# Kernel tuning notes

Hardware: AMD Instinct MI355X
Metric: run time of the kernel (lower is better)

## Reference

```python
import jax, jax.numpy as jnp
import numpy as np

# dims
B, T, N, D = 4, 256, 64, 512
H, DH = 8, 64            # n_head, d_head; H*DH == D
DF = 4 * D               # SwiGLU hidden
EPS = 1e-6


def rmsnorm(x, w):
    return x * jax.lax.rsqrt(jnp.mean(x * x, axis=-1, keepdims=True) + EPS) * w


def phi(x):
    # positive feature map for kernelized (linear) attention ('SMReg' assumed elu+1 style)
    return jax.nn.elu(x) + 1.0


def heads(x):
    return x.reshape(*x.shape[:-1], H, DH)


def lin_att(Xq, Xkv, wq, wk, wv, wo):
    # low-rank high-order linear attention: kernelized attention applied
    # independently along each tensor mode (time T, entities N), averaged.
    q = phi(heads(Xq @ wq))   # [B,T,N,H,DH]
    k = phi(heads(Xkv @ wk))
    v = heads(Xkv @ wv)
    # mode 1 (time): attend over T, batch over (B,N)
    kv_t = jnp.einsum('btnhk,btnhv->bnhkv', k, v)          # [B,N,H,DH,DH]
    ks_t = k.sum(axis=1)                                   # [B,N,H,DH]
    den_t = jnp.einsum('btnhk,bnhk->btnh', q, ks_t) + EPS
    out_t = jnp.einsum('btnhk,bnhkv->btnhv', q, kv_t) / den_t[..., None]
    # mode 2 (entities): attend over N, batch over (B,T)
    kv_n = jnp.einsum('btnhk,btnhv->bthkv', k, v)
    ks_n = k.sum(axis=2)
    den_n = jnp.einsum('btnhk,bthk->btnh', q, ks_n) + EPS
    out_n = jnp.einsum('btnhk,bthkv->btnhv', q, kv_n) / den_n[..., None]
    out = 0.5 * (out_t + out_n)
    return out.reshape(*Xq.shape[:-1], H * DH) @ wo


def swiglu(x, w1, w2, w3):
    return (jax.nn.silu(x @ w1) * (x @ w3)) @ w2


def setup_inputs() -> dict:
    key = jax.random.key(0)
    ks = jax.random.split(key, 20)
    s = 0.02
    inp = {
        'X': jax.random.normal(ks[0], (B, T, N, D), jnp.float32),
        'Z': jax.random.normal(ks[1], (B, T, N, D), jnp.float32),
        'n1': jnp.ones((D,), jnp.float32),
        'n2': jnp.ones((D,), jnp.float32),
        'n3': jnp.ones((D,), jnp.float32),
        'nz': jnp.ones((D,), jnp.float32),
        'a_wq': jax.random.normal(ks[2], (D, H * DH), jnp.float32) * s,
        'a_wk': jax.random.normal(ks[3], (D, H * DH), jnp.float32) * s,
        'a_wv': jax.random.normal(ks[4], (D, H * DH), jnp.float32) * s,
        'a_wo': jax.random.normal(ks[5], (H * DH, D), jnp.float32) * s,
        'c_wq': jax.random.normal(ks[6], (D, H * DH), jnp.float32) * s,
        'c_wk': jax.random.normal(ks[7], (D, H * DH), jnp.float32) * s,
        'c_wv': jax.random.normal(ks[8], (D, H * DH), jnp.float32) * s,
        'c_wo': jax.random.normal(ks[9], (H * DH, D), jnp.float32) * s,
        'f_w1': jax.random.normal(ks[10], (D, DF), jnp.float32) * s,
        'f_w2': jax.random.normal(ks[11], (DF, D), jnp.float32) * s,
        'f_w3': jax.random.normal(ks[12], (D, DF), jnp.float32) * s,
    }
    return inp


def reference(X, Z, n1, n2, n3, nz, a_wq, a_wk, a_wv, a_wo,
              c_wq, c_wk, c_wv, c_wo, f_w1, f_w2, f_w3):
    # h = X + SelfAtt(norm1(X))
    xn = rmsnorm(X, n1)
    h = X + lin_att(xn, xn, a_wq, a_wk, a_wv, a_wo)
    # h = h + CrossAtt(norm3(h), normz(Z))
    h = h + lin_att(rmsnorm(h, n3), rmsnorm(Z, nz), c_wq, c_wk, c_wv, c_wo)
    # out = h + SwiGLU(norm2(h))   (dropout p=0 -> identity)
    return h + swiglu(rmsnorm(h, n2), f_w1, f_w2, f_w3)
```

## Files before the change

### kernel.cpp

```cpp
#include <hip/hip_runtime.h>

typedef short s16x8 __attribute__((ext_vector_type(8)));
typedef float f32x4 __attribute__((ext_vector_type(4)));
typedef unsigned short u16;
typedef unsigned int u32;

__device__ __forceinline__ float bf2f(u16 u) {
  union { unsigned int i; float f; } v; v.i = ((unsigned int)u) << 16; return v.f;
}
__device__ __forceinline__ u16 f2bf(float f) {
  union { float f; unsigned int i; } v; v.f = f;
  unsigned int r = v.i + 0x7fffu + ((v.i >> 16) & 1u);
  return (u16)(r >> 16);
}
__device__ __forceinline__ float bflo(u32 x) {
  union { unsigned int i; float f; } v; v.i = x << 16; return v.f;
}
__device__ __forceinline__ float bfhi(u32 x) {
  union { unsigned int i; float f; } v; v.i = x & 0xffff0000u; return v.f;
}

__device__ __forceinline__ void gload16(const u16* g, u16* l) {
  __builtin_amdgcn_global_load_lds(
      (const __attribute__((address_space(1))) u32*)g,
      (__attribute__((address_space(3))) u32*)l, 16, 0, 0);
}

template<int KDIM, int NDIM>
__launch_bounds__(256)
__global__ void wprep(const float* __restrict__ in, u16* __restrict__ out) {
  __shared__ float t[64][65];
  const int tid = threadIdx.x;
  const int nb = NDIM / 64;
  const int tk0 = (blockIdx.x / nb) * 64;
  const int tn0 = (blockIdx.x % nb) * 64;
#pragma unroll
  for (int i = 0; i < 16; i++) {
    int idx = i * 256 + tid;
    int r = idx >> 6, c = idx & 63;
    t[r][c] = in[(long)(tk0 + r) * NDIM + (tn0 + c)];
  }
  __syncthreads();
#pragma unroll
  for (int i = 0; i < 16; i++) {
    int idx = i * 256 + tid;
    int nn = idx >> 6, kk = idx & 63;
    out[(long)(tn0 + nn) * KDIM + (tk0 + kk)] = f2bf(t[kk][nn]);
  }
}

__launch_bounds__(256)
__global__ void rmsnorm_f32(const float* __restrict__ x, const float* __restrict__ w,
                            u16* __restrict__ out) {
  const long row = (long)blockIdx.x * 4 + (threadIdx.x >> 6);
  const int lane = threadIdx.x & 63;
  const float* xr = x + row * 512 + lane * 8;
  float4 v0 = *(const float4*)xr;
  float4 v1 = *(const float4*)(xr + 4);
  float ss = v0.x*v0.x + v0.y*v0.y + v0.z*v0.z + v0.w*v0.w
           + v1.x*v1.x + v1.y*v1.y + v1.z*v1.z + v1.w*v1.w;
#pragma unroll
  for (int o = 1; o < 64; o <<= 1) ss += __shfl_xor(ss, o);
  float sc = rsqrtf(ss * (1.0f / 512.0f) + 1e-6f);
  const float* wp = w + lane * 8;
  float4 w0 = *(const float4*)wp;
  float4 w1 = *(const float4*)(wp + 4);
  union { u16 u[8]; uint4 v; } o;
  o.u[0] = f2bf(v0.x * sc * w0.x);
  o.u[1] = f2bf(v0.y * sc * w0.y);
  o.u[2] = f2bf(v0.z * sc * w0.z);
  o.u[3] = f2bf(v0.w * sc * w0.w);
  o.u[4] = f2bf(v1.x * sc * w1.x);
  o.u[5] = f2bf(v1.y * sc * w1.y);
  o.u[6] = f2bf(v1.z * sc * w1.z);
  o.u[7] = f2bf(v1.w * sc * w1.w);
  *(uint4*)(out + row * 512 + lane * 8) = o.v;
}

__launch_bounds__(256)
__global__ void rmsnorm_bf16(const u16* __restrict__ x, const float* __restrict__ w,
                             u16* __restrict__ out) {
  const long row = (long)blockIdx.x * 4 + (threadIdx.x >> 6);
  const int lane = threadIdx.x & 63;
  uint4 u = *(const uint4*)(x + row * 512 + lane * 8);
  const u16* us = (const u16*)&u;
  float f[8];
  float ss = 0.f;
#pragma unroll
  for (int j = 0; j < 8; j++) { f[j] = bf2f(us[j]); ss += f[j] * f[j]; }
#pragma unroll
  for (int o = 1; o < 64; o <<= 1) ss += __shfl_xor(ss, o);
  float sc = rsqrtf(ss * (1.0f / 512.0f) + 1e-6f);
  const float* wp = w + lane * 8;
  union { u16 u[8]; uint4 v; } o;
#pragma unroll
  for (int j = 0; j < 8; j++) o.u[j] = f2bf(f[j] * sc * wp[j]);
  *(uint4*)(out + row * 512 + lane * 8) = o.v;
}

enum { EPI_BF16 = 0, EPI_PHI = 1, EPI_RESX = 2, EPI_RESH = 3, EPI_SILUMUL = 4,
       EPI_OUTF = 5, EPI_QKV = 6, EPI_KV = 7 };

template<int KD, int EPI>
__launch_bounds__(256)
__global__ void gemm128(const u16* __restrict__ A, const u16* __restrict__ Bt,
                        void* __restrict__ C0, void* __restrict__ C1,
                        void* __restrict__ C2, const void* __restrict__ aux,
                        int Ns) {
  __shared__ u16 smem[32768];
  u16* Asm = smem;
  u16* Bsm = smem + 16384;
  const int tid = threadIdx.x;
  const int lane = tid & 63;
  const int wv = tid >> 6;
  const int gx = gridDim.x;
  int L = blockIdx.y * gx + blockIdx.x;
  const int cpx = (gx * gridDim.y) >> 3;
  L = (L & 7) * cpx + (L >> 3);
  const long m0 = (long)(L / gx) * 128;
  const int nb = L % gx;
  const long n0 = (long)nb * 128;

  const int wr = (wv >> 1) * 64;
  const int wc = (wv & 1) * 64;
  const int fr = lane & 15;
  const int frq = lane >> 4;

  const int r0 = wv * 32 + (lane >> 3);
  const int sg8 = ((lane & 7) ^ ((lane >> 3) & 7)) * 8;
  const u16* Ag = A + (m0 + r0) * KD + sg8;
  const u16* Bg = Bt + (n0 + r0) * KD + sg8;
  u16* Alds = Asm + wv * 2048;
  u16* Blds = Bsm + wv * 2048;

  f32x4 acc[4][4] = {};

  auto STAGE = [&](int b, int kt) {
    const long k0 = (long)kt * 64;
#pragma unroll
    for (int j = 0; j < 4; j++) {
      gload16(Ag + (long)(j * 8) * KD + k0, Alds + b * 8192 + j * 512);
      gload16(Bg + (long)(j * 8) * KD + k0, Blds + b * 8192 + j * 512);
    }
  };
  auto COMPUTE = [&](int b) {
#pragma unroll
    for (int ks = 0; ks < 2; ks++) {
      const int slot = ((ks * 4 + frq) ^ (fr & 7)) * 8;
      s16x8 af[4], bf[4];
#pragma unroll
      for (int i = 0; i < 4; i++)
        af[i] = *(const s16x8*)&Asm[b * 8192 + (wr + i * 16 + fr) * 64 + slot];
#pragma unroll
      for (int j = 0; j < 4; j++)
        bf[j] = *(const s16x8*)&Bsm[b * 8192 + (wc + j * 16 + fr) * 64 + slot];
#pragma unroll
      for (int i = 0; i < 4; i++)
#pragma unroll
        for (int j = 0; j < 4; j++)
          acc[i][j] = __builtin_amdgcn_mfma_f32_16x16x32_bf16(af[i], bf[j], acc[i][j], 0, 0, 0);
    }
  };

  constexpr int NT = KD / 64;
  STAGE(0, 0);
#pragma unroll 1
  for (int t = 0; t < NT; ++t) {
    if (t + 1 < NT) {
      STAGE((t + 1) & 1, t + 1);
      asm volatile("s_waitcnt vmcnt(8)" ::: "memory");
    } else {
      asm volatile("s_waitcnt vmcnt(0)" ::: "memory");
    }
    __builtin_amdgcn_s_barrier();
    COMPUTE(t & 1);
    asm volatile("s_waitcnt lgkmcnt(0)" ::: "memory");
    __builtin_amdgcn_s_barrier();
  }

  u16* Cs = smem;
  const int col = lane & 15;
  const int rb = frq * 4;
  const int seg = (EPI == EPI_QKV || EPI == EPI_KV) ? (nb >> 2) : 0;
#pragma unroll
  for (int i = 0; i < 4; i++) {
#pragma unroll
    for (int r = 0; r < 4; r++) {
      const int ml = wr + i * 16 + rb + r;
#pragma unroll
      for (int j = 0; j < 4; j++) {
        const int nl = wc + j * 16 + col;
        float v = acc[i][j][r];
        if constexpr (EPI == EPI_PHI) {
          v = v > 0.f ? v + 1.f : __expf(v);
        } else if constexpr (EPI == EPI_QKV) {
          if (seg < 2) v = v > 0.f ? v + 1.f : __expf(v);
        } else if constexpr (EPI == EPI_KV) {
          if (seg == 0) v = v > 0.f ? v + 1.f : __expf(v);
        }
        Cs[ml * 148 + nl] = f2bf(v);
      }
    }
  }
  __syncthreads();

#pragma unroll
  for (int rep = 0; rep < 8; rep++) {
    const int idx = rep * 256 + tid;
    const int row = idx >> 4;
    const int nc = (idx & 15) * 8;
    const long m = m0 + row;
    uint4 vv = *(const uint4*)&Cs[row * 148 + nc];
    const u16* vp = (const u16*)&vv;
    if constexpr (EPI == EPI_QKV) {
      u16* P = (u16*)(seg == 0 ? C0 : (seg == 1 ? C1 : C2));
      *(uint4*)(P + m * 512 + (int)((n0 + nc) & 511)) = vv;
    } else if constexpr (EPI == EPI_KV) {
      u16* P = (u16*)(seg == 0 ? C0 : C1);
      *(uint4*)(P + m * 512 + (int)((n0 + nc) & 511)) = vv;
    } else if constexpr (EPI == EPI_BF16 || EPI == EPI_PHI) {
      *(uint4*)((u16*)C0 + m * Ns + n0 + nc) = vv;
    } else if constexpr (EPI == EPI_RESX) {
      const float* ax = (const float*)aux + m * Ns + n0 + nc;
      float4 a0 = *(const float4*)ax;
      float4 a1 = *(const float4*)(ax + 4);
      union { u16 u[8]; uint4 v; } o;
      o.u[0] = f2bf(a0.x + bf2f(vp[0]));
      o.u[1] = f2bf(a0.y + bf2f(vp[1]));
      o.u[2] = f2bf(a0.z + bf2f(vp[2]));
      o.u[3] = f2bf(a0.w + bf2f(vp[3]));
      o.u[4] = f2bf(a1.x + bf2f(vp[4]));
      o.u[5] = f2bf(a1.y + bf2f(vp[5]));
      o.u[6] = f2bf(a1.z + bf2f(vp[6]));
      o.u[7] = f2bf(a1.w + bf2f(vp[7]));
      *(uint4*)((u16*)C0 + m * Ns + n0 + nc) = o.v;
    } else if constexpr (EPI == EPI_RESH) {
      uint4 hh = *(const uint4*)((const u16*)aux + m * Ns + n0 + nc);
      const u16* hp = (const u16*)&hh;
      union { u16 u[8]; uint4 v; } o;
#pragma unroll
      for (int e = 0; e < 8; e++) o.u[e] = f2bf(bf2f(hp[e]) + bf2f(vp[e]));
      *(uint4*)((u16*)C0 + m * Ns + n0 + nc) = o.v;
    } else if constexpr (EPI == EPI_SILUMUL) {
      uint4 tt = *(const uint4*)((const u16*)aux + m * Ns + n0 + nc);
      const u16* tp = (const u16*)&tt;
      union { u16 u[8]; uint4 v; } o;
#pragma unroll
      for (int e = 0; e < 8; e++) {
        float t2 = bf2f(tp[e]);
        float s = t2 / (1.f + __expf(-t2));
        o.u[e] = f2bf(s * bf2f(vp[e]));
      }
      *(uint4*)((u16*)C0 + m * Ns + n0 + nc) = o.v;
    } else {
      uint4 hh = *(const uint4*)((const u16*)aux + m * Ns + n0 + nc);
      const u16* hp = (const u16*)&hh;
      float* o = (float*)C0 + m * Ns + n0 + nc;
      float4 o0, o1;
      o0.x = bf2f(hp[0]) + bf2f(vp[0]);
      o0.y = bf2f(hp[1]) + bf2f(vp[1]);
      o0.z = bf2f(hp[2]) + bf2f(vp[2]);
      o0.w = bf2f(hp[3]) + bf2f(vp[3]);
      o1.x = bf2f(hp[4]) + bf2f(vp[4]);
      o1.y = bf2f(hp[5]) + bf2f(vp[5]);
      o1.z = bf2f(hp[6]) + bf2f(vp[6]);
      o1.w = bf2f(hp[7]) + bf2f(vp[7]);
      *(float4*)o = o0;
      *(float4*)(o + 4) = o1;
    }
  }
}

__launch_bounds__(256)
__global__ void att_mode1(const u16* __restrict__ q, const u16* __restrict__ k,
                          const u16* __restrict__ v, u16* __restrict__ attc) {
  __shared__ u32 KT[64][132];
  __shared__ u32 VT[64][132];
  __shared__ u16 KVT[64][72];
  __shared__ float ksump[4][64];
  __shared__ float ksum_s[64];
  __shared__ float dinv[256];
  const int tid = threadIdx.x;
  const int lane = tid & 63;
  const int w = tid >> 6;
  const int bnh = blockIdx.x;
  const int h = bnh & 7;
  const int bn = bnh >> 3;
  const int n = bn & 63;
  const int b = bn >> 6;
  const long base = ((long)b * 16384 + n) * 512 + h * 64;
  const int fr = lane & 15;
  const int frq = lane >> 4;
  const int fk = frq * 8;

#pragma unroll
  for (int r = 0; r < 4; r++) {
    const int tp = (tid & 63) + (r & 1) * 64;
    const int c8 = (tid >> 6) + (r >> 1) * 4;
    const long g0 = base + (long)(2 * tp) * 32768 + c8 * 8;
    uint4 ka = *(const uint4*)(k + g0);
    uint4 kb = *(const uint4*)(k + g0 + 32768);
    uint4 va = *(const uint4*)(v + g0);
    uint4 vb = *(const uint4*)(v + g0 + 32768);
    const u16* kap = (const u16*)&ka; const u16* kbp = (const u16*)&kb;
    const u16* vap = (const u16*)&va; const u16* vbp = (const u16*)&vb;
#pragma unroll
    for (int e = 0; e < 8; e++) {
      KT[c8 * 8 + e][tp] = (u32)kap[e] | ((u32)kbp[e] << 16);
      VT[c8 * 8 + e][tp] = (u32)vap[e] | ((u32)vbp[e] << 16);
    }
  }
  __syncthreads();

  {
    const int dk = tid >> 2, qq = tid & 3;
    float s = 0.f;
#pragma unroll
    for (int i = 0; i < 8; i++) {
      uint4 x = *(const uint4*)&KT[dk][qq * 32 + i * 4];
      s += bflo(x.x) + bfhi(x.x) + bflo(x.y) + bfhi(x.y)
         + bflo(x.z) + bfhi(x.z) + bflo(x.w) + bfhi(x.w);
    }
    ksump[qq][dk] = s;
  }

  f32x4 acc[4] = {};
#pragma unroll
  for (int ks = 0; ks < 8; ks++) {
    s16x8 af = *(const s16x8*)&VT[w * 16 + fr][ks * 16 + frq * 4];
    s16x8 bk[4];
#pragma unroll
    for (int j = 0; j < 4; j++)
      bk[j] = *(const s16x8*)&KT[j * 16 + fr][ks * 16 + frq * 4];
#pragma unroll
    for (int j = 0; j < 4; j++)
      acc[j] = __builtin_amdgcn_mfma_f32_16x16x32_bf16(af, bk[j], acc[j], 0, 0, 0);
  }
  __syncthreads();
  {
    const int colL = lane & 15, rb = frq * 4;
#pragma unroll
    for (int j = 0; j < 4; j++)
#pragma unroll
      for (int r = 0; r < 4; r++)
        KVT[w * 16 + rb + r][j * 16 + colL] = f2bf(acc[j][r]);
  }
  if (tid < 64) ksum_s[tid] = ksump[0][tid] + ksump[1][tid] + ksump[2][tid] + ksump[3][tid];
  __syncthreads();
  {
    const u16* qp = q + base + (long)tid * 32768;
    float d = 0.f;
#pragma unroll
    for (int c8 = 0; c8 < 8; c8++) {
      uint4 u = ((const uint4*)qp)[c8];
      const u16* us = (const u16*)&u;
#pragma unroll
      for (int e = 0; e < 8; e++) d += bf2f(us[e]) * ksum_s[c8 * 8 + e];
    }
    dinv[tid] = 0.5f / (d + 1e-6f);
  }
  f32x4 acc2[4][4] = {};
#pragma unroll
  for (int ks = 0; ks < 2; ks++) {
    s16x8 aq[4], bk[4];
#pragma unroll
    for (int i = 0; i < 4; i++)
      aq[i] = *(const s16x8*)(q + base + (long)(w * 64 + i * 16 + fr) * 32768 + ks * 32 + fk);
#pragma unroll
    for (int j = 0; j < 4; j++)
      bk[j] = *(const s16x8*)&KVT[j * 16 + fr][ks * 32 + fk];
#pragma unroll
    for (int i = 0; i < 4; i++)
#pragma unroll
      for (int j = 0; j < 4; j++)
        acc2[i][j] = __builtin_amdgcn_mfma_f32_16x16x32_bf16(aq[i], bk[j], acc2[i][j], 0, 0, 0);
  }
  __syncthreads();
  const int colL = lane & 15, rb = frq * 4;
#pragma unroll
  for (int i = 0; i < 4; i++)
#pragma unroll
    for (int r = 0; r < 4; r++) {
      int t = w * 64 + i * 16 + rb + r;
      float inv = dinv[t];
#pragma unroll
      for (int j = 0; j < 4; j++)
        attc[base + (long)t * 32768 + j * 16 + colL] = f2bf(acc2[i][j][r] * inv);
    }
}

__launch_bounds__(256)
__global__ void att_mode2(const u16* __restrict__ q, const u16* __restrict__ k,
                          const u16* __restrict__ v, u16* __restrict__ attc) {
  __shared__ u32 KT[64][36];
  __shared__ u32 VT[64][36];
  __shared__ u16 KVT[64][72];
  __shared__ float ksump[4][64];
  __shared__ float ksum_s[64];
  __shared__ float dinv[64];
  const int tid = threadIdx.x;
  const int lane = tid & 63;
  const int w = tid >> 6;
  const int bth = blockIdx.x;
  const int h = bth & 7;
  const long bt = bth >> 3;
  const long base = bt * 32768 + h * 64;
  const int fr = lane & 15;
  const int frq = lane >> 4;
  const int fk = frq * 8;

  {
    const int np = tid & 31;
    const int c8 = tid >> 5;
    const long g0 = base + (long)(2 * np) * 512 + c8 * 8;
    uint4 ka = *(const uint4*)(k + g0);
    uint4 kb = *(const uint4*)(k + g0 + 512);
    uint4 va = *(const uint4*)(v + g0);
    uint4 vb = *(const uint4*)(v + g0 + 512);
    const u16* kap = (const u16*)&ka; const u16* kbp = (const u16*)&kb;
    const u16* vap = (const u16*)&va; const u16* vbp = (const u16*)&vb;
#pragma unroll
    for (int e = 0; e < 8; e++) {
      KT[c8 * 8 + e][np] = (u32)kap[e] | ((u32)kbp[e] << 16);
      VT[c8 * 8 + e][np] = (u32)vap[e] | ((u32)vbp[e] << 16);
    }
  }
  __syncthreads();
  {
    const int dk = tid >> 2, qq = tid & 3;
    uint4 x0 = *(const uint4*)&KT[dk][qq * 8];
    uint4 x1 = *(const uint4*)&KT[dk][qq * 8 + 4];
    float s = bflo(x0.x) + bfhi(x0.x) + bflo(x0.y) + bfhi(x0.y)
            + bflo(x0.z) + bfhi(x0.z) + bflo(x0.w) + bfhi(x0.w)
            + bflo(x1.x) + bfhi(x1.x) + bflo(x1.y) + bfhi(x1.y)
            + bflo(x1.z) + bfhi(x1.z) + bflo(x1.w) + bfhi(x1.w);
    ksump[qq][dk] = s;
  }
  f32x4 acc[4] = {};
#pragma unroll
  for (int ks = 0; ks < 2; ks++) {
    s16x8 af = *(const s16x8*)&VT[w * 16 + fr][ks * 16 + frq * 4];
    s16x8 bk[4];
#pragma unroll
    for (int j = 0; j < 4; j++)
      bk[j] = *(const s16x8*)&KT[j * 16 + fr][ks * 16 + frq * 4];
#pragma unroll
    for (int j = 0; j < 4; j++)
      acc[j] = __builtin_amdgcn_mfma_f32_16x16x32_bf16(af, bk[j], acc[j], 0, 0, 0);
  }
  __syncthreads();
  {
    const int colL = lane & 15, rb = frq * 4;
#pragma unroll
    for (int j = 0; j < 4; j++)
#pragma unroll
      for (int r = 0; r < 4; r++)
        KVT[w * 16 + rb + r][j * 16 + colL] = f2bf(acc[j][r]);
  }
  if (tid < 64) ksum_s[tid] = ksump[0][tid] + ksump[1][tid] + ksump[2][tid] + ksump[3][tid];
  __syncthreads();
  if (tid < 64) {
    const u16* qp = q + base + (long)tid * 512;
    float d = 0.f;
#pragma unroll
    for (int c8 = 0; c8 < 8; c8++) {
      uint4 u = ((const uint4*)qp)[c8];
      const u16* us = (const u16*)&u;
#pragma unroll
      for (int e = 0; e < 8; e++) d += bf2f(us[e]) * ksum_s[c8 * 8 + e];
    }
    dinv[tid] = 0.5f / (d + 1e-6f);
  }
  f32x4 acc2[4] = {};
#pragma unroll
  for (int ks = 0; ks < 2; ks++) {
    s16x8 aq, bk[4];
    aq = *(const s16x8*)(q + base + (long)(w * 16 + fr) * 512 + ks * 32 + fk);
#pragma unroll
    for (int j = 0; j < 4; j++)
      bk[j] = *(const s16x8*)&KVT[j * 16 + fr][ks * 32 + fk];
#pragma unroll
    for (int j = 0; j < 4; j++)
      acc2[j] = __builtin_amdgcn_mfma_f32_16x16x32_bf16(aq, bk[j], acc2[j], 0, 0, 0);
  }
  __syncthreads();
  const int colL = lane & 15, rb = frq * 4;
#pragma unroll
  for (int r = 0; r < 4; r++) {
    int nr = w * 16 + rb + r;
    float inv = dinv[nr];
#pragma unroll
    for (int j = 0; j < 4; j++) {
      long o = base + (long)nr * 512 + j * 16 + colL;
      attc[o] = f2bf(bf2f(attc[o]) + acc2[j][r] * inv);
    }
  }
}

extern "C" void kernel_launch(void* const* d_in, const int* in_sizes, int n_in,
                              void* d_out, int out_size, void* d_ws, size_t ws_size,
                              hipStream_t stream) {
  const float* X    = (const float*)d_in[0];
  const float* Z    = (const float*)d_in[1];
  const float* n1   = (const float*)d_in[2];
  const float* n2   = (const float*)d_in[3];
  const float* n3   = (const float*)d_in[4];
  const float* nz   = (const float*)d_in[5];
  const float* a_wq = (const float*)d_in[6];
  const float* a_wk = (const float*)d_in[7];
  const float* a_wv = (const float*)d_in[8];
  const float* a_wo = (const float*)d_in[9];
  const float* c_wq = (const float*)d_in[10];
  const float* c_wk = (const float*)d_in[11];
  const float* c_wv = (const float*)d_in[12];
  const float* c_wo = (const float*)d_in[13];
  const float* f_w1 = (const float*)d_in[14];
  const float* f_w2 = (const float*)d_in[15];
  const float* f_w3 = (const float*)d_in[16];
  float* out = (float*)d_out;
  (void)ws_size; (void)in_sizes; (void)n_in; (void)out_size;

  char* p = (char*)d_ws;
  size_t off = 0;
  auto take = [&](size_t bytes) -> char* {
    char* r = p + off;
    off += (bytes + 255) & ~(size_t)255;
    return r;
  };
  u16* w_aq = (u16*)take(512 * 512 * 2);
  u16* w_ak = (u16*)take(512 * 512 * 2);
  u16* w_av = (u16*)take(512 * 512 * 2);
  u16* w_ao = (u16*)take(512 * 512 * 2);
  u16* w_cq = (u16*)take(512 * 512 * 2);
  u16* w_ck = (u16*)take(512 * 512 * 2);
  u16* w_cv = (u16*)take(512 * 512 * 2);
  u16* w_co = (u16*)take(512 * 512 * 2);
  u16* w_f1 = (u16*)take(2048 * 512 * 2);
  u16* w_f3 = (u16*)take(2048 * 512 * 2);
  u16* w_f2 = (u16*)take(512 * 2048 * 2);
  u16* xn   = (u16*)take((size_t)65536 * 512 * 2);
  u16* hbuf = (u16*)take((size_t)65536 * 512 * 2);
  u16* qbuf = (u16*)take((size_t)65536 * 512 * 2);
  u16* kbuf = (u16*)d_out;
  u16* vbuf = (u16*)d_out + (size_t)65536 * 512;
  u16* attc = xn;
  u16* tslot = qbuf;

  dim3 b256(256);
  dim3 gQKV(12, 512);
  dim3 gKV(8, 512);
  dim3 gP(4, 512);
  dim3 gU(16, 128);
  dim3 gD(4, 128);

  wprep<512, 512><<<64, b256, 0, stream>>>(a_wq, w_aq);
  wprep<512, 512><<<64, b256, 0, stream>>>(a_wk, w_ak);
  wprep<512, 512><<<64, b256, 0, stream>>>(a_wv, w_av);
  wprep<512, 512><<<64, b256, 0, stream>>>(a_wo, w_ao);
  wprep<512, 512><<<64, b256, 0, stream>>>(c_wq, w_cq);
  wprep<512, 512><<<64, b256, 0, stream>>>(c_wk, w_ck);
  wprep<512, 512><<<64, b256, 0, stream>>>(c_wv, w_cv);
  wprep<512, 512><<<64, b256, 0, stream>>>(c_wo, w_co);
  wprep<512, 2048><<<256, b256, 0, stream>>>(f_w1, w_f1);
  wprep<512, 2048><<<256, b256, 0, stream>>>(f_w3, w_f3);
  wprep<2048, 512><<<256, b256, 0, stream>>>(f_w2, w_f2);

  rmsnorm_f32<<<16384, b256, 0, stream>>>(X, n1, xn);
  gemm128<512, EPI_QKV><<<gQKV, b256, 0, stream>>>(xn, w_aq, qbuf, kbuf, vbuf, nullptr, 1536);
  att_mode1<<<2048, b256, 0, stream>>>(qbuf, kbuf, vbuf, attc);
  att_mode2<<<8192, b256, 0, stream>>>(qbuf, kbuf, vbuf, attc);
  gemm128<512, EPI_RESX><<<gP, b256, 0, stream>>>(attc, w_ao, hbuf, nullptr, nullptr, X, 512);

  rmsnorm_bf16<<<16384, b256, 0, stream>>>(hbuf, n3, xn);
  gemm128<512, EPI_PHI><<<gP, b256, 0, stream>>>(xn, w_cq, qbuf, nullptr, nullptr, nullptr, 512);
  rmsnorm_f32<<<16384, b256, 0, stream>>>(Z, nz, xn);
  gemm128<512, EPI_KV><<<gKV, b256, 0, stream>>>(xn, w_ck, kbuf, vbuf, nullptr, nullptr, 1024);
  att_mode1<<<2048, b256, 0, stream>>>(qbuf, kbuf, vbuf, attc);
  att_mode2<<<8192, b256, 0, stream>>>(qbuf, kbuf, vbuf, attc);
  gemm128<512, EPI_RESH><<<gP, b256, 0, stream>>>(attc, w_co, hbuf, nullptr, nullptr, hbuf, 512);

  rmsnorm_bf16<<<16384, b256, 0, stream>>>(hbuf, n2, xn);
  const int CH = 16384;
  for (int c = 0; c < 4; c++) {
    const size_t ro = (size_t)c * CH * 512;
    gemm128<512, EPI_BF16><<<gU, b256, 0, stream>>>(xn + ro, w_f1, tslot, nullptr, nullptr, nullptr, 2048);
    gemm128<512, EPI_SILUMUL><<<gU, b256, 0, stream>>>(xn + ro, w_f3, tslot, nullptr, nullptr, tslot, 2048);
    gemm128<2048, EPI_OUTF><<<gD, b256, 0, stream>>>(tslot, w_f2, out + ro, nullptr, nullptr, hbuf + ro, 512);
  }
}
```

Measured before the change: 1.432 ms.

## Halve GEMM shared memory with K=32 stages and two-pass epilogue for occupancy

```diff
diff --git a/kernel.cpp b/kernel.cpp
--- a/kernel.cpp
+++ b/kernel.cpp
@@ -102,14 +102,12 @@
        EPI_OUTF = 5, EPI_QKV = 6, EPI_KV = 7 };
 
 template<int KD, int EPI>
-__launch_bounds__(256)
+__launch_bounds__(256, 5)
 __global__ void gemm128(const u16* __restrict__ A, const u16* __restrict__ Bt,
                         void* __restrict__ C0, void* __restrict__ C1,
                         void* __restrict__ C2, const void* __restrict__ aux,
                         int Ns) {
-  __shared__ u16 smem[32768];
-  u16* Asm = smem;
-  u16* Bsm = smem + 16384;
+  __shared__ u16 smem[16384];
   const int tid = threadIdx.x;
   const int lane = tid & 63;
   const int wv = tid >> 6;
@@ -126,49 +124,50 @@
   const int fr = lane & 15;
   const int frq = lane >> 4;
 
-  const int r0 = wv * 32 + (lane >> 3);
-  const int sg8 = ((lane & 7) ^ ((lane >> 3) & 7)) * 8;
-  const u16* Ag = A + (m0 + r0) * KD + sg8;
-  const u16* Bg = Bt + (n0 + r0) * KD + sg8;
-  u16* Alds = Asm + wv * 2048;
-  u16* Blds = Bsm + wv * 2048;
+  const int sig = (lane & 7) ^ ((lane >> 3) & 7);
+  const int grow = wv * 32 + 2 * (lane >> 3) + (sig >> 2);
+  const u16* Ag = A + (m0 + grow) * KD + (sig & 3) * 8;
+  const u16* Bg = Bt + (n0 + grow) * KD + (sig & 3) * 8;
 
   f32x4 acc[4][4] = {};
 
   auto STAGE = [&](int b, int kt) {
-    const long k0 = (long)kt * 64;
-#pragma unroll
-    for (int j = 0; j < 4; j++) {
-      gload16(Ag + (long)(j * 8) * KD + k0, Alds + b * 8192 + j * 512);
-      gload16(Bg + (long)(j * 8) * KD + k0, Blds + b * 8192 + j * 512);
-    }
+    const long k0 = (long)kt * 32;
+    gload16(Ag + k0, smem + b * 4096 + wv * 1024);
+    gload16(Ag + (long)16 * KD + k0, smem + b * 4096 + wv * 1024 + 512);
+    gload16(Bg + k0, smem + 8192 + b * 4096 + wv * 1024);
+    gload16(Bg + (long)16 * KD + k0, smem + 8192 + b * 4096 + wv * 1024 + 512);
   };
   auto COMPUTE = [&](int b) {
-#pragma unroll
-    for (int ks = 0; ks < 2; ks++) {
-      const int slot = ((ks * 4 + frq) ^ (fr & 7)) * 8;
-      s16x8 af[4], bf[4];
-#pragma unroll
-      for (int i = 0; i < 4; i++)
-        af[i] = *(const s16x8*)&Asm[b * 8192 + (wr + i * 16 + fr) * 64 + slot];
+    s16x8 af[4], bf[4];
+#pragma unroll
+    for (int i = 0; i < 4; i++) {
+      const int r = wr + i * 16 + fr;
+      const int pr = r >> 1;
+      const int sl = (((r & 1) * 4 + frq) ^ (pr & 7)) * 8;
+      af[i] = *(const s16x8*)&smem[b * 4096 + pr * 64 + sl];
+    }
+#pragma unroll
+    for (int j = 0; j < 4; j++) {
+      const int r = wc + j * 16 + fr;
+      const int pr = r >> 1;
+      const int sl = (((r & 1) * 4 + frq) ^ (pr & 7)) * 8;
+      bf[j] = *(const s16x8*)&smem[8192 + b * 4096 + pr * 64 + sl];
+    }
+#pragma unroll
+    for (int i = 0; i < 4; i++)
 #pragma unroll
       for (int j = 0; j < 4; j++)
-        bf[j] = *(const s16x8*)&Bsm[b * 8192 + (wc + j * 16 + fr) * 64 + slot];
-#pragma unroll
-      for (int i = 0; i < 4; i++)
-#pragma unroll
-        for (int j = 0; j < 4; j++)
-          acc[i][j] = __builtin_amdgcn_mfma_f32_16x16x32_bf16(af[i], bf[j], acc[i][j], 0, 0, 0);
-    }
+        acc[i][j] = __builtin_amdgcn_mfma_f32_16x16x32_bf16(af[i], bf[j], acc[i][j], 0, 0, 0);
   };
 
-  constexpr int NT = KD / 64;
+  constexpr int NT = KD / 32;
   STAGE(0, 0);
 #pragma unroll 1
   for (int t = 0; t < NT; ++t) {
     if (t + 1 < NT) {
       STAGE((t + 1) & 1, t + 1);
-      asm volatile("s_waitcnt vmcnt(8)" ::: "memory");
+      asm volatile("s_waitcnt vmcnt(4)" ::: "memory");
     } else {
       asm volatile("s_waitcnt vmcnt(0)" ::: "memory");
     }
@@ -183,91 +182,96 @@
   const int rb = frq * 4;
   const int seg = (EPI == EPI_QKV || EPI == EPI_KV) ? (nb >> 2) : 0;
 #pragma unroll
-  for (int i = 0; i < 4; i++) {
-#pragma unroll
-    for (int r = 0; r < 4; r++) {
-      const int ml = wr + i * 16 + rb + r;
-#pragma unroll
-      for (int j = 0; j < 4; j++) {
-        const int nl = wc + j * 16 + col;
-        float v = acc[i][j][r];
-        if constexpr (EPI == EPI_PHI) {
-          v = v > 0.f ? v + 1.f : __expf(v);
-        } else if constexpr (EPI == EPI_QKV) {
-          if (seg < 2) v = v > 0.f ? v + 1.f : __expf(v);
-        } else if constexpr (EPI == EPI_KV) {
-          if (seg == 0) v = v > 0.f ? v + 1.f : __expf(v);
+  for (int hh = 0; hh < 2; ++hh) {
+    if ((wv >> 1) == hh) {
+#pragma unroll
+      for (int i = 0; i < 4; i++) {
+#pragma unroll
+        for (int r = 0; r < 4; r++) {
+          const int mloc = i * 16 + rb + r;
+#pragma unroll
+          for (int j = 0; j < 4; j++) {
+            const int nl = wc + j * 16 + col;
+            float v = acc[i][j][r];
+            if constexpr (EPI == EPI_PHI) {
+              v = v > 0.f ? v + 1.f : __expf(v);
+            } else if constexpr (EPI == EPI_QKV) {
+              if (seg < 2) v = v > 0.f ? v + 1.f : __expf(v);
+            } else if constexpr (EPI == EPI_KV) {
+              if (seg == 0) v = v > 0.f ? v + 1.f : __expf(v);
+            }
+            Cs[mloc * 132 + nl] = f2bf(v);
+          }
         }
-        Cs[ml * 148 + nl] = f2bf(v);
       }
     }
-  }
-  __syncthreads();
-
-#pragma unroll
-  for (int rep = 0; rep < 8; rep++) {
-    const int idx = rep * 256 + tid;
-    const int row = idx >> 4;
-    const int nc = (idx & 15) * 8;
-    const long m = m0 + row;
-    uint4 vv = *(const uint4*)&Cs[row * 148 + nc];
-    const u16* vp = (const u16*)&vv;
-    if constexpr (EPI == EPI_QKV) {
-      u16* P = (u16*)(seg == 0 ? C0 : (seg == 1 ? C1 : C2));
-      *(uint4*)(P + m * 512 + (int)((n0 + nc) & 511)) = vv;
-    } else if constexpr (EPI == EPI_KV) {
-      u16* P = (u16*)(seg == 0 ? C0 : C1);
-      *(uint4*)(P + m * 512 + (int)((n0 + nc) & 511)) = vv;
-    } else if constexpr (EPI == EPI_BF16 || EPI == EPI_PHI) {
-      *(uint4*)((u16*)C0 + m * Ns + n0 + nc) = vv;
-    } else if constexpr (EPI == EPI_RESX) {
-      const float* ax = (const float*)aux + m * Ns + n0 + nc;
-      float4 a0 = *(const float4*)ax;
-      float4 a1 = *(const float4*)(ax + 4);
-      union { u16 u[8]; uint4 v; } o;
-      o.u[0] = f2bf(a0.x + bf2f(vp[0]));
-      o.u[1] = f2bf(a0.y + bf2f(vp[1]));
-      o.u[2] = f2bf(a0.z + bf2f(vp[2]));
-      o.u[3] = f2bf(a0.w + bf2f(vp[3]));
-      o.u[4] = f2bf(a1.x + bf2f(vp[4]));
-      o.u[5] = f2bf(a1.y + bf2f(vp[5]));
-      o.u[6] = f2bf(a1.z + bf2f(vp[6]));
-      o.u[7] = f2bf(a1.w + bf2f(vp[7]));
-      *(uint4*)((u16*)C0 + m * Ns + n0 + nc) = o.v;
-    } else if constexpr (EPI == EPI_RESH) {
-      uint4 hh = *(const uint4*)((const u16*)aux + m * Ns + n0 + nc);
-      const u16* hp = (const u16*)&hh;
-      union { u16 u[8]; uint4 v; } o;
-#pragma unroll
-      for (int e = 0; e < 8; e++) o.u[e] = f2bf(bf2f(hp[e]) + bf2f(vp[e]));
-      *(uint4*)((u16*)C0 + m * Ns + n0 + nc) = o.v;
-    } else if constexpr (EPI == EPI_SILUMUL) {
-      uint4 tt = *(const uint4*)((const u16*)aux + m * Ns + n0 + nc);
-      const u16* tp = (const u16*)&tt;
-      union { u16 u[8]; uint4 v; } o;
-#pragma unroll
-      for (int e = 0; e < 8; e++) {
-        float t2 = bf2f(tp[e]);
-        float s = t2 / (1.f + __expf(-t2));
-        o.u[e] = f2bf(s * bf2f(vp[e]));
+    __syncthreads();
+#pragma unroll
+    for (int rep = 0; rep < 4; rep++) {
+      const int idx = rep * 256 + tid;
+      const int row = idx >> 4;
+      const int nc = (idx & 15) * 8;
+      const long m = m0 + hh * 64 + row;
+      uint4 vv = *(const uint4*)&Cs[row * 132 + nc];
+      const u16* vp = (const u16*)&vv;
+      if constexpr (EPI == EPI_QKV) {
+        u16* P = (u16*)(seg == 0 ? C0 : (seg == 1 ? C1 : C2));
+        *(uint4*)(P + m * 512 + (int)((n0 + nc) & 511)) = vv;
+      } else if constexpr (EPI == EPI_KV) {
+        u16* P = (u16*)(seg == 0 ? C0 : C1);
+        *(uint4*)(P + m * 512 + (int)((n0 + nc) & 511)) = vv;
+      } else if constexpr (EPI == EPI_BF16 || EPI == EPI_PHI) {
+        *(uint4*)((u16*)C0 + m * Ns + n0 + nc) = vv;
+      } else if constexpr (EPI == EPI_RESX) {
+        const float* ax = (const float*)aux + m * Ns + n0 + nc;
+        float4 a0 = *(const float4*)ax;
+        float4 a1 = *(const float4*)(ax + 4);
+        union { u16 u[8]; uint4 v; } o;
+        o.u[0] = f2bf(a0.x + bf2f(vp[0]));
+        o.u[1] = f2bf(a0.y + bf2f(vp[1]));
+        o.u[2] = f2bf(a0.z + bf2f(vp[2]));
+        o.u[3] = f2bf(a0.w + bf2f(vp[3]));
+        o.u[4] = f2bf(a1.x + bf2f(vp[4]));
+        o.u[5] = f2bf(a1.y + bf2f(vp[5]));
+        o.u[6] = f2bf(a1.z + bf2f(vp[6]));
+        o.u[7] = f2bf(a1.w + bf2f(vp[7]));
+        *(uint4*)((u16*)C0 + m * Ns + n0 + nc) = o.v;
+      } else if constexpr (EPI == EPI_RESH) {
+        uint4 hhv = *(const uint4*)((const u16*)aux + m * Ns + n0 + nc);
+        const u16* hp = (const u16*)&hhv;
+        union { u16 u[8]; uint4 v; } o;
+#pragma unroll
+        for (int e = 0; e < 8; e++) o.u[e] = f2bf(bf2f(hp[e]) + bf2f(vp[e]));
+        *(uint4*)((u16*)C0 + m * Ns + n0 + nc) = o.v;
+      } else if constexpr (EPI == EPI_SILUMUL) {
+        uint4 tt = *(const uint4*)((const u16*)aux + m * Ns + n0 + nc);
+        const u16* tp = (const u16*)&tt;
+        union { u16 u[8]; uint4 v; } o;
+#pragma unroll
+        for (int e = 0; e < 8; e++) {
+          float t2 = bf2f(tp[e]);
+          float s = t2 / (1.f + __expf(-t2));
+          o.u[e] = f2bf(s * bf2f(vp[e]));
+        }
+        *(uint4*)((u16*)C0 + m * Ns + n0 + nc) = o.v;
+      } else {
+        uint4 hhv = *(const uint4*)((const u16*)aux + m * Ns + n0 + nc);
+        const u16* hp = (const u16*)&hhv;
+        float* o = (float*)C0 + m * Ns + n0 + nc;
+        float4 o0, o1;
+        o0.x = bf2f(hp[0]) + bf2f(vp[0]);
+        o0.y = bf2f(hp[1]) + bf2f(vp[1]);
+        o0.z = bf2f(hp[2]) + bf2f(vp[2]);
+        o0.w = bf2f(hp[3]) + bf2f(vp[3]);
+        o1.x = bf2f(hp[4]) + bf2f(vp[4]);
+        o1.y = bf2f(hp[5]) + bf2f(vp[5]);
+        o1.z = bf2f(hp[6]) + bf2f(vp[6]);
+        o1.w = bf2f(hp[7]) + bf2f(vp[7]);
+        *(float4*)o = o0;
+        *(float4*)(o + 4) = o1;
       }
-      *(uint4*)((u16*)C0 + m * Ns + n0 + nc) = o.v;
-    } else {
-      uint4 hh = *(const uint4*)((const u16*)aux + m * Ns + n0 + nc);
-      const u16* hp = (const u16*)&hh;
-      float* o = (float*)C0 + m * Ns + n0 + nc;
-      float4 o0, o1;
-      o0.x = bf2f(hp[0]) + bf2f(vp[0]);
-      o0.y = bf2f(hp[1]) + bf2f(vp[1]);
-      o0.z = bf2f(hp[2]) + bf2f(vp[2]);
-      o0.w = bf2f(hp[3]) + bf2f(vp[3]);
-      o1.x = bf2f(hp[4]) + bf2f(vp[4]);
-      o1.y = bf2f(hp[5]) + bf2f(vp[5]);
-      o1.z = bf2f(hp[6]) + bf2f(vp[6]);
-      o1.w = bf2f(hp[7]) + bf2f(vp[7]);
-      *(float4*)o = o0;
-      *(float4*)(o + 4) = o1;
-    }
+    }
+    if (hh == 0) __syncthreads();
   }
 }
 
```

New measurement: 1.544 ms. 1.08x slower.

## Add A-panel-resident GEMM kernel that sweeps many N tiles per block

Applied to the files above, without the earlier changes.

```diff
diff --git a/kernel.cpp b/kernel.cpp
--- a/kernel.cpp
+++ b/kernel.cpp
@@ -100,6 +100,198 @@
 
 enum { EPI_BF16 = 0, EPI_PHI = 1, EPI_RESX = 2, EPI_RESH = 3, EPI_SILUMUL = 4,
        EPI_OUTF = 5, EPI_QKV = 6, EPI_KV = 7 };
+
+template<int EPI>
+__launch_bounds__(512, 1)
+__global__ void gemm_ap(const u16* __restrict__ A, const u16* __restrict__ Bt,
+                        void* __restrict__ C0, void* __restrict__ C1,
+                        void* __restrict__ C2, const void* __restrict__ aux,
+                        int Ns, int ntPer) {
+  __shared__ u16 smem[81920];
+  u16* Ap = smem;
+  u16* Bsm = smem + 65536;
+  const int tid = threadIdx.x;
+  const int lane = tid & 63;
+  const int wid = tid >> 6;
+  const int G = gridDim.x * gridDim.y;
+  int L = blockIdx.y * gridDim.x + blockIdx.x;
+  L = (L & 7) * (G >> 3) + (L >> 3);
+  const int my = L / gridDim.x;
+  const int sx = L % gridDim.x;
+  const long m0 = (long)my * 128;
+  const int nt0 = sx * ntPer;
+
+  const int wr = (wid >> 2) * 64;
+  const int wc = (wid & 3) * 32;
+  const int fr = lane & 15;
+  const int frq = lane >> 4;
+
+#pragma unroll
+  for (int mrow = 0; mrow < 16; ++mrow) {
+    const int row = wid * 16 + mrow;
+    const u16* src = A + (m0 + row) * 512 + (long)((lane ^ (row & 7)) * 8);
+    gload16(src, Ap + row * 512);
+  }
+
+  auto STAGE_B = [&](int buf, int nn, int kt) {
+#pragma unroll
+    for (int j = 0; j < 2; ++j) {
+      const int rloc = wid * 16 + j * 8 + (lane >> 3);
+      const u16* src = Bt + ((long)(nn * 128 + rloc)) * 512 + (long)kt * 64
+                       + ((lane & 7) ^ ((lane >> 3) & 7)) * 8;
+      gload16(src, Bsm + buf * 8192 + (wid * 16 + j * 8) * 64);
+    }
+  };
+
+  f32x4 acc[4][2];
+  auto COMPUTE = [&](int buf, int kt) {
+#pragma unroll
+    for (int ks = 0; ks < 2; ++ks) {
+      s16x8 af[4], bf[2];
+#pragma unroll
+      for (int i = 0; i < 4; ++i) {
+        const int row = wr + i * 16 + fr;
+        const int l = kt * 8 + ks * 4 + frq;
+        af[i] = *(const s16x8*)&Ap[row * 512 + (l ^ (row & 7)) * 8];
+      }
+#pragma unroll
+      for (int j = 0; j < 2; ++j) {
+        const int row = wc + j * 16 + fr;
+        bf[j] = *(const s16x8*)&Bsm[buf * 8192 + row * 64 + ((ks * 4 + frq) ^ (row & 7)) * 8];
+      }
+#pragma unroll
+      for (int i = 0; i < 4; ++i)
+#pragma unroll
+        for (int j = 0; j < 2; ++j)
+          acc[i][j] = __builtin_amdgcn_mfma_f32_16x16x32_bf16(af[i], bf[j], acc[i][j], 0, 0, 0);
+    }
+  };
+
+  STAGE_B(0, nt0, 0);
+  asm volatile("s_waitcnt vmcnt(0)" ::: "memory");
+  __builtin_amdgcn_s_barrier();
+
+  int g = 0;
+#pragma unroll 1
+  for (int nn = nt0; nn < nt0 + ntPer; ++nn) {
+#pragma unroll
+    for (int i = 0; i < 4; ++i)
+#pragma unroll
+      for (int j = 0; j < 2; ++j) acc[i][j] = (f32x4){0.f, 0.f, 0.f, 0.f};
+
+#pragma unroll 1
+    for (int kt = 0; kt < 8; ++kt, ++g) {
+      const bool lastAll = (nn == nt0 + ntPer - 1) && (kt == 7);
+      if (!lastAll) {
+        if (kt < 7) STAGE_B((g + 1) & 1, nn, kt + 1);
+        else        STAGE_B((g + 1) & 1, nn + 1, 0);
+        asm volatile("s_waitcnt vmcnt(2)" ::: "memory");
+      } else {
+        asm volatile("s_waitcnt vmcnt(0)" ::: "memory");
+      }
+      __builtin_amdgcn_s_barrier();
+      COMPUTE(g & 1, kt);
+      asm volatile("s_waitcnt lgkmcnt(0)" ::: "memory");
+      __builtin_amdgcn_s_barrier();
+    }
+
+    {
+      u16* Cs = Bsm + ((g - 1) & 1) * 8192;
+      const int seg = (EPI == EPI_QKV || EPI == EPI_KV) ? (nn >> 2) : 0;
+      const long ncb = (EPI == EPI_QKV || EPI == EPI_KV) ? (long)((nn & 3) * 128)
+                                                         : (long)nn * 128;
+#pragma unroll 1
+      for (int half = 0; half < 2; ++half) {
+        if ((wid >> 2) == half) {
+#pragma unroll
+          for (int i = 0; i < 4; ++i)
+#pragma unroll
+            for (int r = 0; r < 4; ++r) {
+              const int rowl = i * 16 + frq * 4 + r;
+#pragma unroll
+              for (int j = 0; j < 2; ++j) {
+                const int coll = wc + j * 16 + fr;
+                float v = acc[i][j][r];
+                bool phi = (EPI == EPI_PHI) || (EPI == EPI_QKV && seg < 2) ||
+                           (EPI == EPI_KV && seg == 0);
+                if (phi) v = v > 0.f ? v + 1.f : __expf(v);
+                Cs[rowl * 128 + (coll ^ (frq << 3))] = f2bf(v);
+              }
+            }
+        }
+        __builtin_amdgcn_s_barrier();
+#pragma unroll
+        for (int rep = 0; rep < 2; ++rep) {
+          const int idx = rep * 512 + tid;
+          const int row = idx >> 4;
+          const int c8 = idx & 15;
+          const int wfrq = (row >> 2) & 3;
+          const long m = m0 + half * 64 + row;
+          const long gc = ncb + (long)((c8 ^ wfrq) * 8);
+          uint4 vv = *(const uint4*)&Cs[row * 128 + c8 * 8];
+          const u16* vp = (const u16*)&vv;
+          if constexpr (EPI == EPI_QKV) {
+            u16* P = (u16*)(seg == 0 ? C0 : (seg == 1 ? C1 : C2));
+            *(uint4*)(P + m * 512 + gc) = vv;
+          } else if constexpr (EPI == EPI_KV) {
+            u16* P = (u16*)(seg == 0 ? C0 : C1);
+            *(uint4*)(P + m * 512 + gc) = vv;
+          } else if constexpr (EPI == EPI_BF16 || EPI == EPI_PHI) {
+            *(uint4*)((u16*)C0 + m * Ns + gc) = vv;
+          } else if constexpr (EPI == EPI_RESX) {
+            const float* ax = (const float*)aux + m * Ns + gc;
+            float4 a0 = *(const float4*)ax;
+            float4 a1 = *(const float4*)(ax + 4);
+            union { u16 u[8]; uint4 v; } o;
+            o.u[0] = f2bf(a0.x + bf2f(vp[0]));
+            o.u[1] = f2bf(a0.y + bf2f(vp[1]));
+            o.u[2] = f2bf(a0.z + bf2f(vp[2]));
+            o.u[3] = f2bf(a0.w + bf2f(vp[3]));
+            o.u[4] = f2bf(a1.x + bf2f(vp[4]));
+            o.u[5] = f2bf(a1.y + bf2f(vp[5]));
+            o.u[6] = f2bf(a1.z + bf2f(vp[6]));
+            o.u[7] = f2bf(a1.w + bf2f(vp[7]));
+            *(uint4*)((u16*)C0 + m * Ns + gc) = o.v;
+          } else if constexpr (EPI == EPI_RESH) {
+            uint4 hh = *(const uint4*)((const u16*)aux + m * Ns + gc);
+            const u16* hp = (const u16*)&hh;
+            union { u16 u[8]; uint4 v; } o;
+#pragma unroll
+            for (int e = 0; e < 8; e++) o.u[e] = f2bf(bf2f(hp[e]) + bf2f(vp[e]));
+            *(uint4*)((u16*)C0 + m * Ns + gc) = o.v;
+          } else if constexpr (EPI == EPI_SILUMUL) {
+            uint4 tt = *(const uint4*)((const u16*)aux + m * Ns + gc);
+            const u16* tp = (const u16*)&tt;
+            union { u16 u[8]; uint4 v; } o;
+#pragma unroll
+            for (int e = 0; e < 8; e++) {
+              float t2 = bf2f(tp[e]);
+              float s = t2 / (1.f + __expf(-t2));
+              o.u[e] = f2bf(s * bf2f(vp[e]));
+            }
+            *(uint4*)((u16*)C0 + m * Ns + gc) = o.v;
+          } else {
+            uint4 hh = *(const uint4*)((const u16*)aux + m * Ns + gc);
+            const u16* hp = (const u16*)&hh;
+            float* o = (float*)C0 + m * Ns + gc;
+            float4 o0, o1;
+            o0.x = bf2f(hp[0]) + bf2f(vp[0]);
+            o0.y = bf2f(hp[1]) + bf2f(vp[1]);
+            o0.z = bf2f(hp[2]) + bf2f(vp[2]);
+            o0.w = bf2f(hp[3]) + bf2f(vp[3]);
+            o1.x = bf2f(hp[4]) + bf2f(vp[4]);
+            o1.y = bf2f(hp[5]) + bf2f(vp[5]);
+            o1.z = bf2f(hp[6]) + bf2f(vp[6]);
+            o1.w = bf2f(hp[7]) + bf2f(vp[7]);
+            *(float4*)o = o0;
+            *(float4*)(o + 4) = o1;
+          }
+        }
+        __builtin_amdgcn_s_barrier();
+      }
+    }
+  }
+}
 
 template<int KD, int EPI>
 __launch_bounds__(256)
@@ -547,10 +739,9 @@
   u16* tslot = qbuf;
 
   dim3 b256(256);
-  dim3 gQKV(12, 512);
-  dim3 gKV(8, 512);
-  dim3 gP(4, 512);
-  dim3 gU(16, 128);
+  dim3 b512(512);
+  dim3 gP(1, 512);
+  dim3 gUc(2, 128);
   dim3 gD(4, 128);
 
   wprep<512, 512><<<64, b256, 0, stream>>>(a_wq, w_aq);
@@ -566,25 +757,25 @@
   wprep<2048, 512><<<256, b256, 0, stream>>>(f_w2, w_f2);
 
   rmsnorm_f32<<<16384, b256, 0, stream>>>(X, n1, xn);
-  gemm128<512, EPI_QKV><<<gQKV, b256, 0, stream>>>(xn, w_aq, qbuf, kbuf, vbuf, nullptr, 1536);
+  gemm_ap<EPI_QKV><<<gP, b512, 0, stream>>>(xn, w_aq, qbuf, kbuf, vbuf, nullptr, 512, 12);
   att_mode1<<<2048, b256, 0, stream>>>(qbuf, kbuf, vbuf, attc);
   att_mode2<<<8192, b256, 0, stream>>>(qbuf, kbuf, vbuf, attc);
-  gemm128<512, EPI_RESX><<<gP, b256, 0, stream>>>(attc, w_ao, hbuf, nullptr, nullptr, X, 512);
+  gemm_ap<EPI_RESX><<<gP, b512, 0, stream>>>(attc, w_ao, hbuf, nullptr, nullptr, X, 512, 4);
 
   rmsnorm_bf16<<<16384, b256, 0, stream>>>(hbuf, n3, xn);
-  gemm128<512, EPI_PHI><<<gP, b256, 0, stream>>>(xn, w_cq, qbuf, nullptr, nullptr, nullptr, 512);
+  gemm_ap<EPI_PHI><<<gP, b512, 0, stream>>>(xn, w_cq, qbuf, nullptr, nullptr, nullptr, 512, 4);
   rmsnorm_f32<<<16384, b256, 0, stream>>>(Z, nz, xn);
-  gemm128<512, EPI_KV><<<gKV, b256, 0, stream>>>(xn, w_ck, kbuf, vbuf, nullptr, nullptr, 1024);
+  gemm_ap<EPI_KV><<<gP, b512, 0, stream>>>(xn, w_ck, kbuf, vbuf, nullptr, nullptr, 512, 8);
   att_mode1<<<2048, b256, 0, stream>>>(qbuf, kbuf, vbuf, attc);
   att_mode2<<<8192, b256, 0, stream>>>(qbuf, kbuf, vbuf, attc);
-  gemm128<512, EPI_RESH><<<gP, b256, 0, stream>>>(attc, w_co, hbuf, nullptr, nullptr, hbuf, 512);
+  gemm_ap<EPI_RESH><<<gP, b512, 0, stream>>>(attc, w_co, hbuf, nullptr, nullptr, hbuf, 512, 4);
 
   rmsnorm_bf16<<<16384, b256, 0, stream>>>(hbuf, n2, xn);
   const int CH = 16384;
   for (int c = 0; c < 4; c++) {
     const size_t ro = (size_t)c * CH * 512;
-    gemm128<512, EPI_BF16><<<gU, b256, 0, stream>>>(xn + ro, w_f1, tslot, nullptr, nullptr, nullptr, 2048);
-    gemm128<512, EPI_SILUMUL><<<gU, b256, 0, stream>>>(xn + ro, w_f3, tslot, nullptr, nullptr, tslot, 2048);
+    gemm_ap<EPI_BF16><<<gUc, b512, 0, stream>>>(xn + ro, w_f1, tslot, nullptr, nullptr, nullptr, 2048, 8);
+    gemm_ap<EPI_SILUMUL><<<gUc, b512, 0, stream>>>(xn + ro, w_f3, tslot, nullptr, nullptr, tslot, 2048, 8);
     gemm128<2048, EPI_OUTF><<<gD, b256, 0, stream>>>(tslot, w_f2, out + ro, nullptr, nullptr, hbuf + ro, 512);
   }
 }
```

New measurement: 1.620 ms. 1.13x slower.
